# Kernel optimization log

Measured on AMD Instinct MI355X. Metric: run time of the kernel, lower is better.

## Reference

```python
import jax, jax.numpy as jnp
import numpy as np

B, SQ, SE = 16, 1024, 1024
C_IN, C_ENC, DK, DV, H = 256, 256, 64, 64, 8
BN_EPS = 1e-5
NEG_SLOPE = 0.01  # torch LeakyReLU default


def setup_inputs() -> dict:
    key = jax.random.key(0)
    ks = jax.random.split(key, 8)
    x = jax.random.normal(ks[0], (B, SE, C_ENC), dtype=jnp.float32)
    q = jax.random.normal(ks[1], (B, SQ, C_IN), dtype=jnp.float32)
    # per-head 1x1-conv projection weights, stacked over heads
    Wq = jax.random.normal(ks[2], (H, DK, C_IN), dtype=jnp.float32) / np.sqrt(C_IN)
    Wk = jax.random.normal(ks[3], (H, DK, C_ENC), dtype=jnp.float32) / np.sqrt(C_ENC)
    Wv = jax.random.normal(ks[4], (H, DV, C_ENC), dtype=jnp.float32) / np.sqrt(C_ENC)
    # output projection (Conv1d(H*DV -> C_IN, k=1, bias=False))
    Wp = jax.random.normal(ks[5], (C_IN, H * DV), dtype=jnp.float32) / np.sqrt(H * DV)
    gamma = jax.random.normal(ks[6], (C_IN,), dtype=jnp.float32) * 0.1 + 1.0
    beta = jax.random.normal(ks[7], (C_IN,), dtype=jnp.float32) * 0.1
    return {"x": x, "q": q, "Wq": Wq, "Wk": Wk, "Wv": Wv, "Wp": Wp,
            "gamma": gamma, "beta": beta}


def reference(x, q, Wq, Wk, Wv, Wp, gamma, beta):
    # per-head Q/K/V via 1x1 conv == einsum over channel dim
    qh = jnp.einsum('bsc,hdc->bhsd', q, Wq)   # [B,H,SQ,DK]
    kh = jnp.einsum('btc,hdc->bhtd', x, Wk)   # [B,H,SE,DK]
    vh = jnp.einsum('btc,hec->bhte', x, Wv)   # [B,H,SE,DV]
    scale = 1.0 / jnp.sqrt(jnp.asarray(DK, dtype=qh.dtype))
    scores = jnp.einsum('bhsd,bhtd->bhst', qh, kh) * scale  # [B,H,SQ,SE]
    attn = jax.nn.softmax(scores, axis=-1)
    oh = jnp.einsum('bhst,bhte->bhse', attn, vh)  # [B,H,SQ,DV]
    # concat heads along feature dim (head-major order, as torch.cat over dim=2)
    o = jnp.transpose(oh, (0, 2, 1, 3)).reshape(B, SQ, H * DV)
    # LBRD projection: 1x1 conv -> BatchNorm1d (train mode: batch stats) -> LeakyReLU
    p = jnp.einsum('bsf,cf->bsc', o, Wp)  # [B,SQ,C_IN]
    mean = jnp.mean(p, axis=(0, 1))        # per-channel over (B, L)
    var = jnp.var(p, axis=(0, 1))          # biased, matching torch BN normalization
    y = (p - mean) * jax.lax.rsqrt(var + BN_EPS) * gamma + beta
    return jnp.where(y >= 0, y, NEG_SLOPE * y)
```

## Files before the change

kernel.cpp:

```cpp
#include <hip/hip_runtime.h>
#include <cstddef>

#define B_    16
#define SQ_   1024
#define SE_   1024
#define CIN_  256
#define DK_   64
#define H_    8
#define HD_   512
#define NROWS 16384
#define BN_EPS 1e-5f
#define NEG_SLOPE 0.01f

typedef __attribute__((ext_vector_type(8))) short bf16x8;
typedef __attribute__((ext_vector_type(4))) float f32x4;

#define BAR()        __builtin_amdgcn_s_barrier()
#define WAIT_LGKM0() asm volatile("s_waitcnt lgkmcnt(0)" ::: "memory")

__device__ __forceinline__ unsigned short f2bf(float f) {
    unsigned int u = __float_as_uint(f);
    return (unsigned short)((u + 0x7FFFu + ((u >> 16) & 1u)) >> 16);
}

#if __has_builtin(__builtin_amdgcn_perm)
__device__ __forceinline__ unsigned int pack_trunc(float lo, float hi) {
    return __builtin_amdgcn_perm(__float_as_uint(hi), __float_as_uint(lo), 0x07060302u);
}
#else
__device__ __forceinline__ unsigned int pack_trunc(float lo, float hi) {
    return (__float_as_uint(lo) >> 16) | (__float_as_uint(hi) & 0xFFFF0000u);
}
#endif

#if __has_builtin(__builtin_amdgcn_exp2f)
#define EXP2F(x) __builtin_amdgcn_exp2f(x)
#else
#define EXP2F(x) exp2f(x)
#endif

__device__ __forceinline__ ushort4 pack4(f32x4 v) {
    ushort4 p;
    p.x = f2bf(v[0]); p.y = f2bf(v[1]);
    p.z = f2bf(v[2]); p.w = f2bf(v[3]);
    return p;
}

__device__ __forceinline__ bf16x8 cvt8(float4 f0, float4 f1) {
    uint4 pk;
    pk.x = pack_trunc(f0.x, f0.y);
    pk.y = pack_trunc(f0.z, f0.w);
    pk.z = pack_trunc(f1.x, f1.y);
    pk.w = pack_trunc(f1.z, f1.w);
    return *(bf16x8*)&pk;
}

__device__ __forceinline__ uint4 cast8_rne(float4 f0, float4 f1, float sc) {
    uint4 pk;
    pk.x = (unsigned)f2bf(f0.x * sc) | ((unsigned)f2bf(f0.y * sc) << 16);
    pk.y = (unsigned)f2bf(f0.z * sc) | ((unsigned)f2bf(f0.w * sc) << 16);
    pk.z = (unsigned)f2bf(f1.x * sc) | ((unsigned)f2bf(f1.y * sc) << 16);
    pk.w = (unsigned)f2bf(f1.z * sc) | ((unsigned)f2bf(f1.w * sc) << 16);
    return pk;
}

__global__ __launch_bounds__(256) void gemm_qkv10(const float* __restrict__ qsrc,
                                                  const float* __restrict__ xsrc,
                                                  const float* __restrict__ Wq,
                                                  const float* __restrict__ Wk,
                                                  const float* __restrict__ Wv,
                                                  unsigned short* __restrict__ qh,
                                                  unsigned short* __restrict__ khb,
                                                  unsigned short* __restrict__ vTb,
                                                  float* __restrict__ stats) {
    __shared__ __align__(16) unsigned short smem[32768];
    unsigned short* Ws = smem;
    unsigned short* Cs = smem;

    const int tid = threadIdx.x;
    const int w = tid >> 6, l = tid & 63, lq = l >> 4, lr = l & 15;

    const int flat = blockIdx.x;
    if (flat < 2) stats[flat * 256 + tid] = 0.f;
    const int xcd  = flat & 7;
    const int jj   = flat >> 3;
    const int bx   = jj % 12;
    const int by   = (jj / 12) + xcd * 16;

    const bool isQ = bx < 4;
    const bool isV = bx >= 8;
    const float* A = isQ ? qsrc : xsrc;
    const float* Wsrc = isQ ? Wq : (isV ? Wv : Wk);
    const int wrow0 = isQ ? bx * 128 : (isV ? (bx - 8) * 128 : (bx - 4) * 128);
    const float wsc = isQ ? 0.18033688011112042f : 1.0f;
    const int n0 = (isQ ? bx : bx - 4) * 128;
    const int m0 = by * 128;

    f32x4 acc[2][8] = {};
    float4 aA[8], aB[8];

    const float* A0 = A + (size_t)(m0 + w * 32 + lr) * 256 + lq * 8;
    const float* A1 = A + (size_t)(m0 + w * 32 + 16 + lr) * 256 + lq * 8;

#define LOAD_A(buf, kstep) do {                                              \
        buf[0] = *(const float4*)(A0 + (kstep) * 64);                        \
        buf[1] = *(const float4*)(A0 + (kstep) * 64 + 4);                    \
        buf[2] = *(const float4*)(A0 + (kstep) * 64 + 32);                   \
        buf[3] = *(const float4*)(A0 + (kstep) * 64 + 36);                   \
        buf[4] = *(const float4*)(A1 + (kstep) * 64);                        \
        buf[5] = *(const float4*)(A1 + (kstep) * 64 + 4);                    \
        buf[6] = *(const float4*)(A1 + (kstep) * 64 + 32);                   \
        buf[7] = *(const float4*)(A1 + (kstep) * 64 + 36);                   \
    } while (0)

#define QKV_STEP(buf, kstep) do {                                            \
        _Pragma("unroll")                                                    \
        for (int ks = 0; ks < 2; ++ks) {                                     \
            bf16x8 a0 = cvt8(buf[ks * 2], buf[ks * 2 + 1]);                  \
            bf16x8 a1 = cvt8(buf[4 + ks * 2], buf[4 + ks * 2 + 1]);          \
            const int colu = (kstep) * 8 + ks * 4 + lq;                      \
            const int cswz = colu ^ (lr & 7);                                \
            if (!isV) {                                                      \
                _Pragma("unroll")                                            \
                for (int j = 0; j < 8; ++j) {                                \
                    bf16x8 bb = *(bf16x8*)&Ws[((j * 16 + lr) * 32 + cswz) * 8]; \
                    acc[0][j] = __builtin_amdgcn_mfma_f32_16x16x32_bf16(bb, a0, acc[0][j], 0, 0, 0); \
                    acc[1][j] = __builtin_amdgcn_mfma_f32_16x16x32_bf16(bb, a1, acc[1][j], 0, 0, 0); \
                }                                                            \
            } else {                                                         \
                _Pragma("unroll")                                            \
                for (int j = 0; j < 8; ++j) {                                \
                    bf16x8 bb = *(bf16x8*)&Ws[((j * 16 + lr) * 32 + cswz) * 8]; \
                    acc[0][j] = __builtin_amdgcn_mfma_f32_16x16x32_bf16(a0, bb, acc[0][j], 0, 0, 0); \
                    acc[1][j] = __builtin_amdgcn_mfma_f32_16x16x32_bf16(a1, bb, acc[1][j], 0, 0, 0); \
                }                                                            \
            }                                                                \
        }                                                                    \
    } while (0)

    LOAD_A(aA, 0);

    #pragma unroll
    for (int i = 0; i < 16; ++i) {
        int u = tid + i * 256;
        int row = u >> 5, colu = u & 31;
        const float* ws = Wsrc + (size_t)(wrow0 + row) * 256 + colu * 8;
        float4 f0 = *(const float4*)(ws);
        float4 f1 = *(const float4*)(ws + 4);
        uint4 pk = cast8_rne(f0, f1, wsc);
        *(uint4*)&Ws[(row * 32 + (colu ^ (row & 7))) * 8] = pk;
    }
    __syncthreads();

    LOAD_A(aB, 1);
    QKV_STEP(aA, 0);
    LOAD_A(aA, 2);
    QKV_STEP(aB, 1);
    LOAD_A(aB, 3);
    QKV_STEP(aA, 2);
    QKV_STEP(aB, 3);

#undef LOAD_A
#undef QKV_STEP

    __syncthreads();
    const int c16 = tid & 15;
    const int rb  = tid >> 4;
    if (!isV) {
        #pragma unroll
        for (int mf = 0; mf < 2; ++mf)
            #pragma unroll
            for (int j = 0; j < 8; ++j)
                *(ushort4*)&Cs[(w * 32 + mf * 16 + lr) * 144 + j * 16 + lq * 4] =
                    pack4(acc[mf][j]);
        __syncthreads();
        unsigned short* C = isQ ? qh : khb;
        #pragma unroll
        for (int it = 0; it < 8; ++it) {
            int r = it * 16 + rb;
            *(uint4*)(C + (size_t)(m0 + r) * 512 + n0 + c16 * 8) =
                *(const uint4*)(Cs + r * 144 + c16 * 8);
        }
    } else {
        #pragma unroll
        for (int mf = 0; mf < 2; ++mf)
            #pragma unroll
            for (int j = 0; j < 8; ++j)
                *(ushort4*)&Cs[(j * 16 + lr) * 144 + w * 32 + mf * 16 + lq * 4] =
                    pack4(acc[mf][j]);
        __syncthreads();
        const int bb = m0 >> 10, t0 = m0 & 1023;
        #pragma unroll
        for (int it = 0; it < 8; ++it) {
            int el = it * 16 + rb;
            int colv = n0 - 512 + el;
            int hh = colv >> 6, e = colv & 63;
            *(uint4*)(vTb + (size_t)((bb * 8 + hh) * 64 + e) * 1024 + t0 + c16 * 8) =
                *(const uint4*)(Cs + el * 144 + c16 * 8);
        }
    }
}

__global__ __launch_bounds__(256) void attn_mfma12(const unsigned short* __restrict__ qh,
                                                   const unsigned short* __restrict__ kh,
                                                   const unsigned short* __restrict__ vT,
                                                   unsigned short* __restrict__ o) {
    __shared__ __align__(16) unsigned short Ks[64 * 64];
    __shared__ __align__(16) unsigned short Vs[64 * 64];
    __shared__ __align__(16) unsigned short Ps[4][64 * 40];

    const int tid = threadIdx.x;
    const int w = tid >> 6, l = tid & 63, lq = l >> 4, lr = l & 15;

    const int flat = blockIdx.x;
    const int xcd  = flat & 7;
    const int jj   = flat >> 3;
    const int q0   = (jj & 3) * 256;
    const int hb   = (jj >> 2) + xcd * 16;
    const int h    = hb & 7;
    const int b    = hb >> 3;

    const int swz = (lr & 7) << 3;

    bf16x8 qf[4][2];
    #pragma unroll
    for (int mm = 0; mm < 4; ++mm) {
        const unsigned short* qr =
            qh + (size_t)(b * SQ_ + q0 + w * 64 + mm * 16 + lr) * HD_ + h * DK_;
        qf[mm][0] = *(const bf16x8*)(qr + lq * 8);
        qf[mm][1] = *(const bf16x8*)(qr + 32 + lq * 8);
    }

    const unsigned short* kb = kh + (size_t)(b * SE_) * HD_ + h * DK_;
    const unsigned short* vb = vT + (size_t)((b * 8 + h) * 64) * 1024;

    const int se = tid >> 3;
    const int sc = (tid & 7) * 8;
    const int sswz = (se & 7) << 3;

    float l_i[4] = {};
    f32x4 oacc[4][4] = {};
    unsigned short* Pw = Ps[w];

    uint4 kR[2], vR[2];
    #pragma unroll
    for (int ps = 0; ps < 2; ++ps) {
        int rr = se + ps * 32;
        kR[ps] = *(const uint4*)(kb + (size_t)rr * HD_ + sc);
        vR[ps] = *(const uint4*)(vb + (size_t)rr * 1024 + sc);
    }

    for (int t0 = 0; t0 < SE_; t0 += 64) {
        BAR();
        #pragma unroll
        for (int ps = 0; ps < 2; ++ps) {
            int rr = se + ps * 32;
            int ad = ((rr * 64 + sc) ^ sswz);
            *(uint4*)&Ks[ad] = kR[ps];
            *(uint4*)&Vs[ad] = vR[ps];
        }
        if (t0 + 64 < SE_) {
            #pragma unroll
            for (int ps = 0; ps < 2; ++ps) {
                int rr = se + ps * 32;
                kR[ps] = *(const uint4*)(kb + (size_t)(t0 + 64 + rr) * HD_ + sc);
                vR[ps] = *(const uint4*)(vb + (size_t)rr * 1024 + t0 + 64 + sc);
            }
        }
        WAIT_LGKM0();
        BAR();

        f32x4 s0[2][4] = {};
        __builtin_amdgcn_s_setprio(1);
        #pragma unroll
        for (int ks = 0; ks < 2; ++ks)
            #pragma unroll
            for (int tt = 0; tt < 2; ++tt) {
                bf16x8 kf = *(bf16x8*)&Ks[((tt * 16 + lr) * 64 + ks * 32 + lq * 8) ^ swz];
                #pragma unroll
                for (int mm = 0; mm < 4; ++mm)
                    s0[tt][mm] = __builtin_amdgcn_mfma_f32_16x16x32_bf16(kf, qf[mm][ks], s0[tt][mm], 0, 0, 0);
            }
        __builtin_amdgcn_s_setprio(0);

        #pragma unroll
        for (int mm = 0; mm < 4; ++mm)
            #pragma unroll
            for (int tt = 0; tt < 2; ++tt) {
                float e0 = EXP2F(s0[tt][mm][0]);
                float e1 = EXP2F(s0[tt][mm][1]);
                float e2 = EXP2F(s0[tt][mm][2]);
                float e3 = EXP2F(s0[tt][mm][3]);
                l_i[mm] += (e0 + e1) + (e2 + e3);
                uint2 pk;
                pk.x = pack_trunc(e0, e1);
                pk.y = pack_trunc(e2, e3);
                *(uint2*)&Pw[(mm * 16 + lr) * 40 + tt * 16 + lq * 4] = pk;
            }

        f32x4 s1[2][4] = {};
        __builtin_amdgcn_s_setprio(1);
        #pragma unroll
        for (int ks = 0; ks < 2; ++ks)
            #pragma unroll
            for (int tt = 0; tt < 2; ++tt) {
                bf16x8 kf = *(bf16x8*)&Ks[(((tt + 2) * 16 + lr) * 64 + ks * 32 + lq * 8) ^ swz];
                #pragma unroll
                for (int mm = 0; mm < 4; ++mm)
                    s1[tt][mm] = __builtin_amdgcn_mfma_f32_16x16x32_bf16(kf, qf[mm][ks], s1[tt][mm], 0, 0, 0);
            }
        __builtin_amdgcn_s_setprio(0);

        asm volatile("s_waitcnt lgkmcnt(0)" ::: "memory");

        __builtin_amdgcn_s_setprio(1);
        {
            bf16x8 pf[4];
            #pragma unroll
            for (int mm = 0; mm < 4; ++mm)
                pf[mm] = *(bf16x8*)&Pw[(mm * 16 + lr) * 40 + lq * 8];
            #pragma unroll
            for (int j = 0; j < 4; ++j) {
                bf16x8 vf = *(bf16x8*)&Vs[((j * 16 + lr) * 64 + lq * 8) ^ swz];
                #pragma unroll
                for (int mm = 0; mm < 4; ++mm)
                    oacc[mm][j] = __builtin_amdgcn_mfma_f32_16x16x32_bf16(vf, pf[mm], oacc[mm][j], 0, 0, 0);
            }
        }
        __builtin_amdgcn_s_setprio(0);

        #pragma unroll
        for (int mm = 0; mm < 4; ++mm)
            #pragma unroll
            for (int tt = 0; tt < 2; ++tt) {
                float e0 = EXP2F(s1[tt][mm][0]);
                float e1 = EXP2F(s1[tt][mm][1]);
                float e2 = EXP2F(s1[tt][mm][2]);
                float e3 = EXP2F(s1[tt][mm][3]);
                l_i[mm] += (e0 + e1) + (e2 + e3);
                uint2 pk;
                pk.x = pack_trunc(e0, e1);
                pk.y = pack_trunc(e2, e3);
                *(uint2*)&Pw[(mm * 16 + lr) * 40 + tt * 16 + lq * 4] = pk;
            }

        asm volatile("s_waitcnt lgkmcnt(0)" ::: "memory");

        __builtin_amdgcn_s_setprio(1);
        {
            bf16x8 pf[4];
            #pragma unroll
            for (int mm = 0; mm < 4; ++mm)
                pf[mm] = *(bf16x8*)&Pw[(mm * 16 + lr) * 40 + lq * 8];
            #pragma unroll
            for (int j = 0; j < 4; ++j) {
                bf16x8 vf = *(bf16x8*)&Vs[((j * 16 + lr) * 64 + 32 + lq * 8) ^ swz];
                #pragma unroll
                for (int mm = 0; mm < 4; ++mm)
                    oacc[mm][j] = __builtin_amdgcn_mfma_f32_16x16x32_bf16(vf, pf[mm], oacc[mm][j], 0, 0, 0);
            }
        }
        __builtin_amdgcn_s_setprio(0);
    }

    float inv[4];
    #pragma unroll
    for (int mm = 0; mm < 4; ++mm) {
        float t = l_i[mm];
        t += __shfl_xor(t, 16);
        t += __shfl_xor(t, 32);
        inv[mm] = 1.0f / t;
    }

    #pragma unroll
    for (int mm = 0; mm < 4; ++mm)
        #pragma unroll
        for (int j = 0; j < 4; ++j) {
            f32x4 v = oacc[mm][j];
            v[0] *= inv[mm]; v[1] *= inv[mm]; v[2] *= inv[mm]; v[3] *= inv[mm];
            *(ushort4*)&o[(size_t)(b * SQ_ + q0 + w * 64 + mm * 16 + lr) * HD_ +
                          h * DK_ + j * 16 + lq * 4] = pack4(v);
        }
}

__global__ __launch_bounds__(256) void gemm_out4(const unsigned short* __restrict__ A,
                                                 const float* __restrict__ Wp,
                                                 float* __restrict__ C,
                                                 float* __restrict__ gsum,
                                                 float* __restrict__ gsumsq) {
    __shared__ __align__(16) unsigned short Ws[32768];
    const int tid = threadIdx.x;
    const int w = tid >> 6, l = tid & 63, lq = l >> 4, lr = l & 15;

    const int flat = blockIdx.x;
    const int xcd  = flat & 7;
    const int jj   = flat >> 3;
    const int bx   = jj & 3;
    const int by   = (jj >> 2) + xcd * 16;
    const int n0 = bx * 64, m0 = by * 128;
    const int K = 512;

    f32x4 acc[2][4] = {};
    uint4 aA[4], aB[4];

    const unsigned short* A0 = A + (size_t)(m0 + w * 32 + lr) * K + lq * 8;
    const unsigned short* A1 = A + (size_t)(m0 + w * 32 + 16 + lr) * K + lq * 8;

#define LOADO(buf, kstep) do {                                               \
        buf[0] = *(const uint4*)(A0 + (kstep) * 64);                         \
        buf[1] = *(const uint4*)(A0 + (kstep) * 64 + 32);                    \
        buf[2] = *(const uint4*)(A1 + (kstep) * 64);                         \
        buf[3] = *(const uint4*)(A1 + (kstep) * 64 + 32);                    \
    } while (0)

#define OSTEP(buf, kstep) do {                                               \
        _Pragma("unroll")                                                    \
        for (int ks = 0; ks < 2; ++ks) {                                     \
            bf16x8 a0 = *(bf16x8*)&buf[ks];                                  \
            bf16x8 a1 = *(bf16x8*)&buf[2 + ks];                              \
            const int cu = (kstep) * 8 + ks * 4 + lq;                        \
            const int cswz = cu ^ (lr & 7);                                  \
            _Pragma("unroll")                                                \
            for (int j = 0; j < 4; ++j) {                                    \
                bf16x8 bb = *(bf16x8*)&Ws[((j * 16 + lr) * 64 + cswz) * 8];  \
                acc[0][j] = __builtin_amdgcn_mfma_f32_16x16x32_bf16(a0, bb, acc[0][j], 0, 0, 0); \
                acc[1][j] = __builtin_amdgcn_mfma_f32_16x16x32_bf16(a1, bb, acc[1][j], 0, 0, 0); \
            }                                                                \
        }                                                                    \
    } while (0)

    LOADO(aA, 0);

    #pragma unroll
    for (int i = 0; i < 16; ++i) {
        int u = tid + i * 256;
        int row = u >> 6, cu = u & 63;
        const float* ws = Wp + (size_t)(n0 + row) * 512 + cu * 8;
        float4 f0 = *(const float4*)(ws);
        float4 f1 = *(const float4*)(ws + 4);
        uint4 pk = cast8_rne(f0, f1, 1.0f);
        *(uint4*)&Ws[(row * 64 + (cu ^ (row & 7))) * 8] = pk;
    }
    __syncthreads();

    LOADO(aB, 1); OSTEP(aA, 0);
    LOADO(aA, 2); OSTEP(aB, 1);
    LOADO(aB, 3); OSTEP(aA, 2);
    LOADO(aA, 4); OSTEP(aB, 3);
    LOADO(aB, 5); OSTEP(aA, 4);
    LOADO(aA, 6); OSTEP(aB, 5);
    LOADO(aB, 7); OSTEP(aA, 6);
    OSTEP(aB, 7);

#undef LOADO
#undef OSTEP

    float cs[4] = {}, cq[4] = {};
    #pragma unroll
    for (int m = 0; m < 2; ++m)
        #pragma unroll
        for (int j = 0; j < 4; ++j)
            #pragma unroll
            for (int r = 0; r < 4; ++r) {
                float v = acc[m][j][r];
                C[(size_t)(m0 + w * 32 + m * 16 + lq * 4 + r) * 256 + n0 + j * 16 + lr] = v;
                cs[j] += v;
                cq[j] += v * v;
            }
    #pragma unroll
    for (int j = 0; j < 4; ++j) {
        cs[j] += __shfl_xor(cs[j], 16); cs[j] += __shfl_xor(cs[j], 32);
        cq[j] += __shfl_xor(cq[j], 16); cq[j] += __shfl_xor(cq[j], 32);
    }
    __syncthreads();
    float* red = (float*)Ws;
    if (lq == 0) {
        #pragma unroll
        for (int j = 0; j < 4; ++j) {
            red[w * 128 + j * 16 + lr]      = cs[j];
            red[w * 128 + 64 + j * 16 + lr] = cq[j];
        }
    }
    __syncthreads();
    if (tid < 128) {
        int col = tid & 63, stat = tid >> 6;
        float t = red[stat * 64 + col] + red[128 + stat * 64 + col] +
                  red[256 + stat * 64 + col] + red[384 + stat * 64 + col];
        atomicAdd((stat ? gsumsq : gsum) + n0 + col, t);
    }
}

__global__ __launch_bounds__(256) void bn_norm4(const float* __restrict__ p,
                                                const float* __restrict__ gsum,
                                                const float* __restrict__ gsumsq,
                                                const float* __restrict__ gamma,
                                                const float* __restrict__ beta,
                                                float* __restrict__ out) {
    int i = blockIdx.x * 256 + threadIdx.x;
    int c0 = (i * 4) & 255;
    const float invN = 1.0f / (float)NROWS;
    float4 pv = *(const float4*)(p + (size_t)i * 4);
    float vals[4] = {pv.x, pv.y, pv.z, pv.w};
    float res[4];
    #pragma unroll
    for (int k = 0; k < 4; ++k) {
        int c = c0 + k;
        float mean = gsum[c] * invN;
        float var  = gsumsq[c] * invN - mean * mean;
        float v = (vals[k] - mean) * rsqrtf(var + BN_EPS) * gamma[c] + beta[c];
        res[k] = v >= 0.f ? v : NEG_SLOPE * v;
    }
    float4 ov = {res[0], res[1], res[2], res[3]};
    *(float4*)(out + (size_t)i * 4) = ov;
}

extern "C" void kernel_launch(void* const* d_in, const int* in_sizes, int n_in,
                              void* d_out, int out_size, void* d_ws, size_t ws_size,
                              hipStream_t stream) {
    const float* x     = (const float*)d_in[0];
    const float* q     = (const float*)d_in[1];
    const float* Wq    = (const float*)d_in[2];
    const float* Wk    = (const float*)d_in[3];
    const float* Wv    = (const float*)d_in[4];
    const float* Wp    = (const float*)d_in[5];
    const float* gamma = (const float*)d_in[6];
    const float* beta  = (const float*)d_in[7];
    float* out = (float*)d_out;

    char* base = (char*)d_ws;
    unsigned short* qh   = (unsigned short*)(base + 1048576);
    unsigned short* khb  = (unsigned short*)(base + 17825792);
    unsigned short* vTb  = (unsigned short*)(base + 34603008);
    unsigned short* ob   = (unsigned short*)(base + 51380224);
    float*          pbuf = (float*)        (base + 68157440);
    float*          stats= (float*)        (base + 84934656);

    gemm_qkv10<<<1536, 256, 0, stream>>>(q, x, Wq, Wk, Wv, qh, khb, vTb, stats);

    attn_mfma12<<<512, 256, 0, stream>>>(qh, khb, vTb, ob);

    gemm_out4<<<512, 256, 0, stream>>>(ob, Wp, pbuf, stats, stats + 256);

    bn_norm4<<<4096, 256, 0, stream>>>(pbuf, stats, stats + 256, gamma, beta, out);
}
```

Before: 204.1 us.

## Fuse BatchNorm apply into output GEMM via cooperative grid sync

The output-projection GEMM no longer writes the pre-norm activations to a workspace buffer. It accumulates the per-channel sums, does a grid-wide sync through a cooperative launch, and then applies BatchNorm and LeakyReLU straight from its register accumulators. This removes one 16 MB fp32 write and read plus a kernel launch. In exchange, all 512 blocks must be co-resident with 64 KB of shared memory each, and the kernel pays for a grid barrier. The stores also become less coalesced scalar writes.

```diff
diff --git a/kernel.cpp b/kernel.cpp
--- a/kernel.cpp
+++ b/kernel.cpp
@@ -1,5 +1,8 @@
 #include <hip/hip_runtime.h>
+#include <hip/hip_cooperative_groups.h>
 #include <cstddef>
+
+namespace cg = cooperative_groups;
 
 #define B_    16
 #define SQ_   1024
@@ -383,9 +386,11 @@
         }
 }
 
-__global__ __launch_bounds__(256) void gemm_out4(const unsigned short* __restrict__ A,
+__global__ __launch_bounds__(256) void gemm_out5(const unsigned short* __restrict__ A,
                                                  const float* __restrict__ Wp,
-                                                 float* __restrict__ C,
+                                                 const float* __restrict__ gamma,
+                                                 const float* __restrict__ beta,
+                                                 float* __restrict__ out,
                                                  float* __restrict__ gsum,
                                                  float* __restrict__ gsumsq) {
     __shared__ __align__(16) unsigned short Ws[32768];
@@ -463,7 +468,6 @@
             #pragma unroll
             for (int r = 0; r < 4; ++r) {
                 float v = acc[m][j][r];
-                C[(size_t)(m0 + w * 32 + m * 16 + lq * 4 + r) * 256 + n0 + j * 16 + lr] = v;
                 cs[j] += v;
                 cq[j] += v * v;
             }
@@ -488,30 +492,27 @@
                   red[256 + stat * 64 + col] + red[384 + stat * 64 + col];
         atomicAdd((stat ? gsumsq : gsum) + n0 + col, t);
     }
-}
-
-__global__ __launch_bounds__(256) void bn_norm4(const float* __restrict__ p,
-                                                const float* __restrict__ gsum,
-                                                const float* __restrict__ gsumsq,
-                                                const float* __restrict__ gamma,
-                                                const float* __restrict__ beta,
-                                                float* __restrict__ out) {
-    int i = blockIdx.x * 256 + threadIdx.x;
-    int c0 = (i * 4) & 255;
+
+    __threadfence();
+    cg::this_grid().sync();
+
     const float invN = 1.0f / (float)NROWS;
-    float4 pv = *(const float4*)(p + (size_t)i * 4);
-    float vals[4] = {pv.x, pv.y, pv.z, pv.w};
-    float res[4];
-    #pragma unroll
-    for (int k = 0; k < 4; ++k) {
-        int c = c0 + k;
+    #pragma unroll
+    for (int j = 0; j < 4; ++j) {
+        int c = n0 + j * 16 + lr;
         float mean = gsum[c] * invN;
         float var  = gsumsq[c] * invN - mean * mean;
-        float v = (vals[k] - mean) * rsqrtf(var + BN_EPS) * gamma[c] + beta[c];
-        res[k] = v >= 0.f ? v : NEG_SLOPE * v;
-    }
-    float4 ov = {res[0], res[1], res[2], res[3]};
-    *(float4*)(out + (size_t)i * 4) = ov;
+        float rs   = rsqrtf(var + BN_EPS);
+        float g    = gamma[c], bb = beta[c];
+        #pragma unroll
+        for (int m = 0; m < 2; ++m)
+            #pragma unroll
+            for (int r = 0; r < 4; ++r) {
+                float v = (acc[m][j][r] - mean) * rs * g + bb;
+                v = v >= 0.f ? v : NEG_SLOPE * v;
+                out[(size_t)(m0 + w * 32 + m * 16 + lq * 4 + r) * 256 + c] = v;
+            }
+    }
 }
 
 extern "C" void kernel_launch(void* const* d_in, const int* in_sizes, int n_in,
@@ -532,14 +533,19 @@
     unsigned short* khb  = (unsigned short*)(base + 17825792);
     unsigned short* vTb  = (unsigned short*)(base + 34603008);
     unsigned short* ob   = (unsigned short*)(base + 51380224);
-    float*          pbuf = (float*)        (base + 68157440);
     float*          stats= (float*)        (base + 84934656);
 
     gemm_qkv10<<<1536, 256, 0, stream>>>(q, x, Wq, Wk, Wv, qh, khb, vTb, stats);
 
     attn_mfma12<<<512, 256, 0, stream>>>(qh, khb, vTb, ob);
 
-    gemm_out4<<<512, 256, 0, stream>>>(ob, Wp, pbuf, stats, stats + 256);
-
-    bn_norm4<<<4096, 256, 0, stream>>>(pbuf, stats, stats + 256, gamma, beta, out);
-}
+    {
+        const unsigned short* obc = ob;
+        float* gsum_p = stats;
+        float* gsumsq_p = stats + 256;
+        void* args[] = {(void*)&obc, (void*)&Wp, (void*)&gamma, (void*)&beta,
+                        (void*)&out, (void*)&gsum_p, (void*)&gsumsq_p};
+        hipLaunchCooperativeKernel((const void*)gemm_out5, dim3(512), dim3(256),
+                                   args, 0, stream);
+    }
+}
```

Result: slower. 275.3 us (+34.9%).
